# Optimization experiments

Hardware: AMD Instinct MI355X
Metric: run time of the kernel (lower is better)

Reference implementation:

```python
import jax, jax.numpy as jnp
import numpy as np

MODEL_DIM = 1024
NUM_HEADS = 16
HEAD_DIM = MODEL_DIM // NUM_HEADS
ROPE_THETA = 10000.0


def _rotate_half(x):
    x1, x2 = jnp.split(x, 2, axis=-1)
    return jnp.concatenate((-x2, x1), axis=-1)


def _rope_cos_sin(seq_len, dtype):
    inv_freq = 1.0 / (ROPE_THETA ** (jnp.arange(0, HEAD_DIM, 2, dtype=jnp.float32) / HEAD_DIM))
    pos = jnp.arange(seq_len, dtype=jnp.float32)
    freqs = jnp.einsum('i,j->ij', pos, inv_freq)  # [S, HEAD_DIM/2]
    emb = jnp.concatenate((freqs, freqs), axis=-1)  # [S, HEAD_DIM]
    return jnp.cos(emb).astype(dtype), jnp.sin(emb).astype(dtype)


def setup_inputs() -> dict:
    key = jax.random.key(0)
    ks = jax.random.split(key, 9)
    B, S, D = 4, 2048, MODEL_DIM
    scale = 1.0 / np.sqrt(D)
    inp = {
        'x': jax.random.normal(ks[0], (B, S, D), dtype=jnp.float32),
        'key_padding_mask': jnp.ones((B, S), dtype=bool),
        'wq': jax.random.normal(ks[1], (D, D), dtype=jnp.float32) * scale,
        'bq': jnp.zeros((D,), dtype=jnp.float32),
        'wk': jax.random.normal(ks[2], (D, D), dtype=jnp.float32) * scale,
        'bk': jnp.zeros((D,), dtype=jnp.float32),
        'wv': jax.random.normal(ks[3], (D, D), dtype=jnp.float32) * scale,
        'bv': jnp.zeros((D,), dtype=jnp.float32),
        'wo': jax.random.normal(ks[4], (D, D), dtype=jnp.float32) * scale,
        'bo': jnp.zeros((D,), dtype=jnp.float32),
    }
    return inp


def reference(x, key_padding_mask, wq, bq, wk, bk, wv, bv, wo, bo):
    B, S, D = x.shape
    H, Hd = NUM_HEADS, HEAD_DIM
    q = (x @ wq + bq).reshape(B, S, H, Hd).transpose(0, 2, 1, 3)
    k = (x @ wk + bk).reshape(B, S, H, Hd).transpose(0, 2, 1, 3)
    v = (x @ wv + bv).reshape(B, S, H, Hd).transpose(0, 2, 1, 3)
    cos, sin = _rope_cos_sin(S, x.dtype)  # [S, Hd]
    cos = cos[None, None]
    sin = sin[None, None]
    q = q * cos + _rotate_half(q) * sin
    k = k * cos + _rotate_half(k) * sin
    scores = jnp.einsum('bhqd,bhkd->bhqk', q, k) / jnp.sqrt(jnp.asarray(Hd, x.dtype))
    mask = key_padding_mask[:, None, None, :]
    scores = jnp.where(mask, scores, jnp.finfo(scores.dtype).min)
    attn = jax.nn.softmax(scores, axis=-1)
    ctx = jnp.einsum('bhqk,bhkd->bhqd', attn, v)
    ctx = ctx.transpose(0, 2, 1, 3).reshape(B, S, D)
    out = ctx @ wo + bo
    out = out * key_padding_mask[:, :, None].astype(out.dtype)
    return out
```

## Files before the change

### kernel.cpp

```cpp
#include <hip/hip_runtime.h>
#include <math.h>

#define S_LEN  2048
#define NH     16
#define HD     64
#define DMODEL 1024
#define BATCH  4
#define M_TOK  (BATCH * S_LEN)

typedef __bf16 bf16x8 __attribute__((ext_vector_type(8)));
typedef float  floatx4 __attribute__((ext_vector_type(4)));
typedef float  floatx16 __attribute__((ext_vector_type(16)));

typedef __attribute__((address_space(1))) const void cg_void;
typedef __attribute__((address_space(3))) void lds_void;

#if __has_builtin(__builtin_amdgcn_exp2f)
#define EXP2(x) __builtin_amdgcn_exp2f(x)
#else
#define EXP2(x) exp2f(x)
#endif

__device__ __forceinline__ void gload16(const void* g, void* l) {
    __builtin_amdgcn_global_load_lds((cg_void*)g, (lds_void*)l, 16, 0, 0);
}

__device__ __forceinline__ unsigned short f2bf(float f) {
    unsigned int u = __builtin_bit_cast(unsigned int, f);
    u = (u + 0x7FFF + ((u >> 16) & 1)) >> 16;
    return (unsigned short)u;
}

__device__ __forceinline__ unsigned cvtpk(float lo, float hi) {
    unsigned r;
    asm volatile("v_cvt_pk_bf16_f32 %0, %1, %2" : "=v"(r) : "v"(lo), "v"(hi));
    return r;
}

__device__ __forceinline__ void swap32(unsigned &a, unsigned &b) {
    asm volatile("v_permlane32_swap_b32 %0, %1" : "+v"(a), "+v"(b));
}

__device__ __forceinline__ float max3f(float a, float b, float c) {
    float r;
    asm("v_max3_f32 %0, %1, %2, %3" : "=v"(r) : "v"(a), "v"(b), "v"(c));
    return r;
}

__global__ __launch_bounds__(256)
void prep_kernel(const float* __restrict__ x,
                 const float* __restrict__ wq, const float* __restrict__ wk,
                 const float* __restrict__ wv, const float* __restrict__ wo,
                 const int* __restrict__ mask,
                 unsigned short* __restrict__ xb, unsigned short* __restrict__ wstack,
                 unsigned short* __restrict__ wto,
                 float* __restrict__ cs, float* __restrict__ sn,
                 float* __restrict__ biasG, int* __restrict__ flags)
{
    __shared__ float tile[32][33];
    const int blk = blockIdx.x;
    const int tid = threadIdx.x;
    constexpr size_t WSZ = (size_t)DMODEL * DMODEL;

    if (blk < 8192) {
        const int idx = blk * 256 + tid;
        float4 a = *reinterpret_cast<const float4*>(&x[(size_t)idx * 4]);
        ushort4 o;
        o.x = f2bf(a.x); o.y = f2bf(a.y); o.z = f2bf(a.z); o.w = f2bf(a.w);
        *reinterpret_cast<ushort4*>(&xb[(size_t)idx * 4]) = o;
    } else if (blk < 12288) {
        const int rel = blk - 8192;
        const int mat = rel >> 10;
        const float* w = (mat == 0) ? wq : (mat == 1) ? wk : (mat == 2) ? wv : wo;
        unsigned short* wt = (mat < 3) ? (wstack + (size_t)mat * WSZ) : wto;
        const int rel10 = rel & 1023;
        const int n0 = (rel10 & 31) * 32;
        const int k0 = (rel10 >> 5) * 32;
        const int tx  = tid & 31;
        const int ty8 = tid >> 5;
        #pragma unroll
        for (int i = 0; i < 4; ++i)
            tile[ty8 + i * 8][tx] = w[(size_t)(k0 + ty8 + i * 8) * DMODEL + n0 + tx];
        __syncthreads();
        #pragma unroll
        for (int i = 0; i < 4; ++i)
            wt[(size_t)(n0 + ty8 + i * 8) * DMODEL + k0 + tx] = f2bf(tile[tx][ty8 + i * 8]);
    } else if (blk < 12544) {
        const int idx = (blk - 12288) * 256 + tid;
        const int j = idx & 31;
        const int s = idx >> 5;
        double invf = pow(10000.0, -(double)j / 32.0);
        double a = (double)s * invf;
        cs[idx] = (float)cos(a);
        sn[idx] = (float)sin(a);
    } else {
        for (int i = tid; i < BATCH * S_LEN; i += 256) {
            const int b = i >> 11, r = i & 2047;
            const int kt = r >> 6, rem = r & 63;
            const int hig = rem >> 5, kbb = (rem >> 4) & 1, reg = rem & 15;
            const int key = kt * 64 + kbb * 32 + hig * 4 + (reg & 3) + ((reg >> 2) << 3);
            biasG[i] = mask[b * S_LEN + key] ? 0.0f : -3.0e38f;
        }
        for (int i = tid; i < BATCH * 32; i += 256) {
            const int b = i >> 5, kt = i & 31;
            int ok = 1;
            for (int j = 0; j < 64; ++j) ok &= (mask[b * S_LEN + kt * 64 + j] != 0);
            flags[i] = ok;
        }
    }
}

__global__ __launch_bounds__(256)
void gemm_qkv(const unsigned short* __restrict__ A, const unsigned short* __restrict__ Bt,
              const float* __restrict__ bq, const float* __restrict__ bk,
              const float* __restrict__ bv,
              const float* __restrict__ cs, const float* __restrict__ sn,
              unsigned short* __restrict__ qbf, unsigned short* __restrict__ kbf,
              unsigned short* __restrict__ vtb)
{
    constexpr int K = DMODEL;
    __shared__ unsigned short As[2][128 * 32];
    __shared__ unsigned short Bs[2][128 * 32];

    const int tid  = threadIdx.x;
    const int lane = tid & 63;
    const int w    = tid >> 6;
    const int wm   = w >> 1;
    const int wn   = w & 1;

    {
    }
    const int gx   = gridDim.x;
    int lin = blockIdx.y * gx + blockIdx.x;
    const int cpx = (gx * gridDim.y) >> 3;
    lin = (lin & 7) * cpx + (lin >> 3);
    const int row0 = (lin / gx) * 128;
    const int col0 = (lin % gx) * 128;

    const int sr  = lane >> 2;
    const int sk8 = (lane & 3) * 8;
    const int fr  = lane & 15;
    const int fk  = (lane >> 4) * 8;

    floatx4 acc[4][4] = {};

    #pragma unroll
    for (int t = 0; t < 2; ++t) {
        const int chunk = w * 32 + t * 16;
        gload16(A  + (size_t)(row0 + chunk + sr) * K + sk8, &As[0][chunk * 32]);
        gload16(Bt + (size_t)(col0 + chunk + sr) * K + sk8, &Bs[0][chunk * 32]);
    }

    for (int kt = 0; kt < K / 32; ++kt) {
        __syncthreads();
        if (kt + 1 < K / 32) {
            const int nb = (kt + 1) & 1;
            const int k0 = (kt + 1) * 32;
            #pragma unroll
            for (int t = 0; t < 2; ++t) {
                const int chunk = w * 32 + t * 16;
                gload16(A  + (size_t)(row0 + chunk + sr) * K + k0 + sk8, &As[nb][chunk * 32]);
                gload16(Bt + (size_t)(col0 + chunk + sr) * K + k0 + sk8, &Bs[nb][chunk * 32]);
            }
        }
        const int cur = kt & 1;
        bf16x8 av[4], bv4[4];
        #pragma unroll
        for (int m = 0; m < 4; ++m)
            av[m] = *reinterpret_cast<const bf16x8*>(&As[cur][(wm * 64 + m * 16 + fr) * 32 + fk]);
        #pragma unroll
        for (int n = 0; n < 4; ++n)
            bv4[n] = *reinterpret_cast<const bf16x8*>(&Bs[cur][(wn * 64 + n * 16 + fr) * 32 + fk]);
        #pragma unroll
        for (int m = 0; m < 4; ++m)
            #pragma unroll
            for (int n = 0; n < 4; ++n)
                acc[m][n] = __builtin_amdgcn_mfma_f32_16x16x32_bf16(av[m], bv4[n], acc[m][n], 0, 0, 0);
    }

    const int rbase = lane >> 4;
    const int sect  = col0 >> 10;
    const int c0    = col0 & 1023;

    if (sect == 2) {
        #pragma unroll
        for (int m = 0; m < 4; ++m)
            #pragma unroll
            for (int n = 0; n < 4; ++n) {
                const int c  = c0 + wn * 64 + n * 16 + fr;
                const int hh = c >> 6, d = c & 63;
                const int mr0 = row0 + wm * 64 + m * 16 + rbase * 4;
                const int bb = mr0 >> 11, ss = mr0 & (S_LEN - 1);
                const float bc = bv[c];
                ushort4 pk4;
                pk4.x = f2bf(acc[m][n][0] + bc);
                pk4.y = f2bf(acc[m][n][1] + bc);
                pk4.z = f2bf(acc[m][n][2] + bc);
                pk4.w = f2bf(acc[m][n][3] + bc);
                *reinterpret_cast<ushort4*>(
                    &vtb[((size_t)(bb * NH + hh) * HD + d) * S_LEN + ss]) = pk4;
            }
    } else {
        unsigned short* outp = sect ? kbf : qbf;
        const float* bias = sect ? bk : bq;
        const float sc = sect ? 1.0f : 0.125f * 1.44269504088896f;
        #pragma unroll
        for (int m = 0; m < 4; ++m)
            #pragma unroll
            for (int n = 0; n < 2; ++n) {
                const int c  = c0 + wn * 64 + n * 16 + fr;
                const int hh = c >> 6, d = c & 63;
                const float b1 = bias[c], b2 = bias[c + 32];
                #pragma unroll
                for (int r = 0; r < 4; ++r) {
                    const int mr = row0 + wm * 64 + m * 16 + rbase * 4 + r;
                    const int bb = mr >> 11, ss = mr & (S_LEN - 1);
                    const float v1 = acc[m][n][r] + b1;
                    const float v2 = acc[m][n + 2][r] + b2;
                    const float co = cs[ss * 32 + d];
                    const float si = sn[ss * 32 + d];
                    const size_t base = ((size_t)(bb * NH + hh) * S_LEN + ss) * HD + d;
                    outp[base]      = f2bf((v1 * co - v2 * si) * sc);
                    outp[base + 32] = f2bf((v2 * co + v1 * si) * sc);
                }
            }
    }
}

__global__ __launch_bounds__(256)
void attn_mfma2(const unsigned short* __restrict__ qbf,
                const unsigned short* __restrict__ kbf,
                const unsigned short* __restrict__ vtb,
                const float* __restrict__ biasG,
                const int* __restrict__ flags,
                unsigned short* __restrict__ ctxb)
{
    __shared__ unsigned short Ks[2][64 * 64];
    __shared__ unsigned short Vs[2][64 * 64];

    const int tid  = threadIdx.x;
    const int lane = tid & 63;
    const int w    = tid >> 6;
    const int bh   = blockIdx.x;
    const int b    = bh >> 4;
    const int h    = bh & 15;
    const int q0   = blockIdx.y * 128 + w * 32;
    const size_t hb = (size_t)bh * S_LEN * HD;

    const int lo5 = lane & 31;
    const int hi5 = lane >> 5;
    const int srow   = lane >> 3;
    const int schunk = (lane & 7) ^ srow;

    bf16x8 qf[4];
    #pragma unroll
    for (int ks = 0; ks < 4; ++ks)
        qf[ks] = *reinterpret_cast<const bf16x8*>(
            &qbf[hb + (size_t)(q0 + lo5) * HD + ks * 16 + hi5 * 8]);

    floatx16 oacc[2];
    #pragma unroll
    for (int v = 0; v < 2; ++v)
        #pragma unroll
        for (int i = 0; i < 16; ++i) oacc[v][i] = 0.0f;
    float mrow = -3.0e38f, lrow = 0.0f;

    #define STAGE(KT, BUF)                                                                  \
        _Pragma("unroll")                                                                   \
        for (int t = 0; t < 2; ++t) {                                                       \
            const int r0 = w * 16 + t * 8;                                                  \
            gload16(kbf + hb + (size_t)((KT) * 64 + r0 + srow) * HD + schunk * 8,           \
                    &Ks[BUF][r0 * 64]);                                                     \
            gload16(vtb + ((size_t)bh * HD + r0 + srow) * S_LEN + (KT) * 64 + schunk * 8,   \
                    &Vs[BUF][r0 * 64]);                                                     \
        }

    STAGE(0, 0)

    for (int kt = 0; kt < S_LEN / 64; ++kt) {
        __syncthreads();
        if (kt + 1 < S_LEN / 64) { STAGE(kt + 1, (kt + 1) & 1) }
        const int cur = kt & 1;

        floatx16 sacc[2];
        if (flags[b * 32 + kt]) {
            #pragma unroll
            for (int kb = 0; kb < 2; ++kb)
                #pragma unroll
                for (int i = 0; i < 16; ++i) sacc[kb][i] = 0.0f;
        } else {
            const float4* bp = reinterpret_cast<const float4*>(
                &biasG[(size_t)(b * 32 + kt) * 64 + hi5 * 32]);
            #pragma unroll
            for (int kb = 0; kb < 2; ++kb)
                #pragma unroll
                for (int t = 0; t < 4; ++t) {
                    const float4 b4 = bp[kb * 4 + t];
                    sacc[kb][t * 4 + 0] = b4.x; sacc[kb][t * 4 + 1] = b4.y;
                    sacc[kb][t * 4 + 2] = b4.z; sacc[kb][t * 4 + 3] = b4.w;
                }
        }

        __builtin_amdgcn_s_setprio(1);
        #pragma unroll
        for (int kb = 0; kb < 2; ++kb) {
            #pragma unroll
            for (int ks = 0; ks < 4; ++ks) {
                const bf16x8 ak = *reinterpret_cast<const bf16x8*>(
                    (const char*)&Ks[cur][0] + (kb * 32 + lo5) * 128 +
                    ((ks * 32 + hi5 * 16) ^ ((lo5 & 7) << 4)));
                sacc[kb] = __builtin_amdgcn_mfma_f32_32x32x16_bf16(ak, qf[ks], sacc[kb], 0, 0, 0);
            }
        }
        __builtin_amdgcn_s_setprio(0);

        float r0 = max3f(sacc[0][0],  sacc[0][1],  sacc[0][2]);
        float r1 = max3f(sacc[0][3],  sacc[0][4],  sacc[0][5]);
        float r2 = max3f(sacc[0][6],  sacc[0][7],  sacc[0][8]);
        float r3 = max3f(sacc[0][9],  sacc[0][10], sacc[0][11]);
        float r4 = max3f(sacc[0][12], sacc[0][13], sacc[0][14]);
        float r5 = max3f(sacc[1][0],  sacc[1][1],  sacc[1][2]);
        float r6 = max3f(sacc[1][3],  sacc[1][4],  sacc[1][5]);
        float r7 = max3f(sacc[1][6],  sacc[1][7],  sacc[1][8]);
        float r8 = max3f(sacc[1][9],  sacc[1][10], sacc[1][11]);
        float r9 = max3f(sacc[1][12], sacc[1][13], sacc[1][14]);
        float s1 = max3f(r0, r1, r2);
        float s2 = max3f(r3, r4, r5);
        float s3 = max3f(r6, r7, r8);
        float s4 = max3f(r9, sacc[0][15], sacc[1][15]);
        float pmax = fmaxf(max3f(s1, s2, s3), s4);
        pmax = fmaxf(pmax, __shfl_xor(pmax, 32));

        if (!__all(pmax <= mrow + 8.0f)) {
            const float mnew = fmaxf(mrow, pmax);
            const float fscale = EXP2(mrow - mnew);
            mrow = mnew;
            lrow *= fscale;
            #pragma unroll
            for (int v = 0; v < 2; ++v)
                #pragma unroll
                for (int i = 0; i < 16; ++i) oacc[v][i] *= fscale;
        }

        float rs0 = 0.0f, rs1 = 0.0f, rs2 = 0.0f, rs3 = 0.0f;
        #pragma unroll
        for (int kb = 0; kb < 2; ++kb)
            #pragma unroll
            for (int i = 0; i < 16; i += 4) {
                float p0 = EXP2(sacc[kb][i + 0] - mrow);
                float p1 = EXP2(sacc[kb][i + 1] - mrow);
                float p2 = EXP2(sacc[kb][i + 2] - mrow);
                float p3 = EXP2(sacc[kb][i + 3] - mrow);
                sacc[kb][i + 0] = p0; sacc[kb][i + 1] = p1;
                sacc[kb][i + 2] = p2; sacc[kb][i + 3] = p3;
                rs0 += p0; rs1 += p1; rs2 += p2; rs3 += p3;
            }
        float rs = (rs0 + rs1) + (rs2 + rs3);
        rs += __shfl_xor(rs, 32);
        lrow += rs;

        unsigned U0[8], U1[8];
        #pragma unroll
        for (int kb = 0; kb < 2; ++kb)
            #pragma unroll
            for (int s = 0; s < 4; ++s) {
                U0[kb * 4 + s] = cvtpk(sacc[kb][4 * s + 0], sacc[kb][4 * s + 1]);
                U1[kb * 4 + s] = cvtpk(sacc[kb][4 * s + 2], sacc[kb][4 * s + 3]);
            }
        union PF { unsigned u[4]; bf16x8 v; };
        PF pf[4];
        #pragma unroll
        for (int ks = 0; ks < 4; ++ks) {
            unsigned a0 = U0[2 * ks], b0 = U0[2 * ks + 1];
            swap32(a0, b0);
            unsigned a1 = U1[2 * ks], b1 = U1[2 * ks + 1];
            swap32(a1, b1);
            pf[ks].u[0] = a0; pf[ks].u[1] = a1;
            pf[ks].u[2] = b0; pf[ks].u[3] = b1;
        }

        __builtin_amdgcn_s_setprio(1);
        #pragma unroll
        for (int vb = 0; vb < 2; ++vb) {
            #pragma unroll
            for (int ks = 0; ks < 4; ++ks) {
                const bf16x8 av = *reinterpret_cast<const bf16x8*>(
                    (const char*)&Vs[cur][0] + (vb * 32 + lo5) * 128 +
                    ((ks * 32 + hi5 * 16) ^ ((lo5 & 7) << 4)));
                oacc[vb] = __builtin_amdgcn_mfma_f32_32x32x16_bf16(av, pf[ks].v, oacc[vb], 0, 0, 0);
            }
        }
        __builtin_amdgcn_s_setprio(0);
    }

    const float inv = 1.0f / lrow;
    unsigned short* dst = &ctxb[((size_t)b * S_LEN + q0 + lo5) * DMODEL + h * HD];
    #pragma unroll
    for (int vb = 0; vb < 2; ++vb)
        #pragma unroll
        for (int s = 0; s < 4; ++s) {
            const int d0 = vb * 32 + s * 8 + hi5 * 4;
            ushort4 o4;
            o4.x = f2bf(oacc[vb][4 * s + 0] * inv);
            o4.y = f2bf(oacc[vb][4 * s + 1] * inv);
            o4.z = f2bf(oacc[vb][4 * s + 2] * inv);
            o4.w = f2bf(oacc[vb][4 * s + 3] * inv);
            *reinterpret_cast<ushort4*>(&dst[d0]) = o4;
        }
    #undef STAGE
}

__global__ __launch_bounds__(256)
void gemm_out(const unsigned short* __restrict__ A, const unsigned short* __restrict__ Bt,
              const float* __restrict__ bias, const int* __restrict__ mask,
              float* __restrict__ C)
{
    constexpr int K = DMODEL;
    __shared__ unsigned short As[2][128 * 32];
    __shared__ unsigned short Bs[2][128 * 32];

    const int tid  = threadIdx.x;
    const int lane = tid & 63;
    const int w    = tid >> 6;
    const int wm   = w >> 1;
    const int wn   = w & 1;

    const int gx   = gridDim.x;
    int lin = blockIdx.y * gx + blockIdx.x;
    const int cpx = (gx * gridDim.y) >> 3;
    lin = (lin & 7) * cpx + (lin >> 3);
    const int row0 = (lin >> 3) * 128;
    const int col0 = (lin & 7) * 128;

    const int sr  = lane >> 2;
    const int sk8 = (lane & 3) * 8;
    const int fr  = lane & 15;
    const int fk  = (lane >> 4) * 8;

    floatx4 acc[4][4] = {};

    #pragma unroll
    for (int t = 0; t < 2; ++t) {
        const int chunk = w * 32 + t * 16;
        gload16(A  + (size_t)(row0 + chunk + sr) * K + sk8, &As[0][chunk * 32]);
        gload16(Bt + (size_t)(col0 + chunk + sr) * K + sk8, &Bs[0][chunk * 32]);
    }

    for (int kt = 0; kt < K / 32; ++kt) {
        __syncthreads();
        if (kt + 1 < K / 32) {
            const int nb = (kt + 1) & 1;
            const int k0 = (kt + 1) * 32;
            #pragma unroll
            for (int t = 0; t < 2; ++t) {
                const int chunk = w * 32 + t * 16;
                gload16(A  + (size_t)(row0 + chunk + sr) * K + k0 + sk8, &As[nb][chunk * 32]);
                gload16(Bt + (size_t)(col0 + chunk + sr) * K + k0 + sk8, &Bs[nb][chunk * 32]);
            }
        }
        const int cur = kt & 1;
        bf16x8 av[4], bv4[4];
        #pragma unroll
        for (int m = 0; m < 4; ++m)
            av[m] = *reinterpret_cast<const bf16x8*>(&As[cur][(wm * 64 + m * 16 + fr) * 32 + fk]);
        #pragma unroll
        for (int n = 0; n < 4; ++n)
            bv4[n] = *reinterpret_cast<const bf16x8*>(&Bs[cur][(wn * 64 + n * 16 + fr) * 32 + fk]);
        #pragma unroll
        for (int m = 0; m < 4; ++m)
            #pragma unroll
            for (int n = 0; n < 4; ++n)
                acc[m][n] = __builtin_amdgcn_mfma_f32_16x16x32_bf16(av[m], bv4[n], acc[m][n], 0, 0, 0);
    }

    const int rbase = lane >> 4;
    #pragma unroll
    for (int m = 0; m < 4; ++m)
        #pragma unroll
        for (int n = 0; n < 4; ++n) {
            const int c = col0 + wn * 64 + n * 16 + fr;
            const float bc = bias[c];
            #pragma unroll
            for (int r = 0; r < 4; ++r) {
                const int mr = row0 + wm * 64 + m * 16 + rbase * 4 + r;
                C[(size_t)mr * DMODEL + c] = mask[mr] ? (acc[m][n][r] + bc) : 0.0f;
            }
        }
}

extern "C" void kernel_launch(void* const* d_in, const int* in_sizes, int n_in,
                              void* d_out, int out_size, void* d_ws, size_t ws_size,
                              hipStream_t stream) {
    const float* x    = (const float*)d_in[0];
    const int*   mask = (const int*)d_in[1];
    const float* wq = (const float*)d_in[2];
    const float* bq = (const float*)d_in[3];
    const float* wk = (const float*)d_in[4];
    const float* bk = (const float*)d_in[5];
    const float* wv = (const float*)d_in[6];
    const float* bv = (const float*)d_in[7];
    const float* wo = (const float*)d_in[8];
    const float* bo = (const float*)d_in[9];
    float* out = (float*)d_out;

    const size_t QKV = (size_t)M_TOK * DMODEL;
    const size_t WSZ = (size_t)DMODEL * DMODEL;
    unsigned short* xb     = (unsigned short*)d_ws;
    unsigned short* wstack = xb + QKV;
    unsigned short* wto    = wstack + 3 * WSZ;
    unsigned short* qbf    = wto + WSZ;
    unsigned short* kbf    = qbf + QKV;
    unsigned short* vtb    = kbf + QKV;
    unsigned short* ctxb   = vtb + QKV;
    float* cs    = (float*)(ctxb + QKV);
    float* sn    = cs + (size_t)S_LEN * 32;
    float* biasG = sn + (size_t)S_LEN * 32;
    int*   flags = (int*)(biasG + (size_t)BATCH * S_LEN);

    prep_kernel<<<12545, 256, 0, stream>>>(x, wq, wk, wv, wo, mask,
                                           xb, wstack, wto, cs, sn, biasG, flags);

    dim3 qkvgrid(3 * DMODEL / 128, M_TOK / 128);
    gemm_qkv<<<qkvgrid, 256, 0, stream>>>(xb, wstack, bq, bk, bv, cs, sn, qbf, kbf, vtb);

    dim3 agrid(BATCH * NH, S_LEN / 128);
    attn_mfma2<<<agrid, 256, 0, stream>>>(qbf, kbf, vtb, biasG, flags, ctxb);

    dim3 ogrid(DMODEL / 128, M_TOK / 128);
    gemm_out<<<ogrid, 256, 0, stream>>>(ctxb, wto, bo, mask, out);
}
```

Before: 341.5 us.

## Use 512-thread attention blocks with 4-stage K/V pipeline and bitmask flags

The attention kernel now runs 8 waves per block covering 256 queries, so each K/V tile loaded into LDS is shared by twice as many query rows. The double buffer becomes a 4-deep ring with loads issued two tiles ahead and explicit vmcnt waits plus raw barriers in place of __syncthreads. Per-tile mask flags are packed into one 32-bit word per batch and read once. The RoPE table is computed in float instead of double, which is cheaper in the prep kernel but slightly less precise. The trade-offs are twice the LDS per block, a halved grid (fewer blocks to spread across CUs), and waitcnt counts that must match the outstanding loads exactly.

```diff
diff --git a/kernel.cpp b/kernel.cpp
--- a/kernel.cpp
+++ b/kernel.cpp
@@ -55,9 +55,10 @@
                  unsigned short* __restrict__ xb, unsigned short* __restrict__ wstack,
                  unsigned short* __restrict__ wto,
                  float* __restrict__ cs, float* __restrict__ sn,
-                 float* __restrict__ biasG, int* __restrict__ flags)
+                 float* __restrict__ biasG, unsigned* __restrict__ flagmask)
 {
     __shared__ float tile[32][33];
+    __shared__ unsigned fm[4];
     const int blk = blockIdx.x;
     const int tid = threadIdx.x;
     constexpr size_t WSZ = (size_t)DMODEL * DMODEL;
@@ -89,10 +90,10 @@
         const int idx = (blk - 12288) * 256 + tid;
         const int j = idx & 31;
         const int s = idx >> 5;
-        double invf = pow(10000.0, -(double)j / 32.0);
-        double a = (double)s * invf;
-        cs[idx] = (float)cos(a);
-        sn[idx] = (float)sin(a);
+        const float invf = exp2f(-(float)j * (13.287712379549449f / 32.0f));
+        const float a = (float)s * invf;
+        cs[idx] = cosf(a);
+        sn[idx] = sinf(a);
     } else {
         for (int i = tid; i < BATCH * S_LEN; i += 256) {
             const int b = i >> 11, r = i & 2047;
@@ -101,12 +102,16 @@
             const int key = kt * 64 + kbb * 32 + hig * 4 + (reg & 3) + ((reg >> 2) << 3);
             biasG[i] = mask[b * S_LEN + key] ? 0.0f : -3.0e38f;
         }
+        if (tid < 4) fm[tid] = 0;
+        __syncthreads();
         for (int i = tid; i < BATCH * 32; i += 256) {
             const int b = i >> 5, kt = i & 31;
             int ok = 1;
             for (int j = 0; j < 64; ++j) ok &= (mask[b * S_LEN + kt * 64 + j] != 0);
-            flags[i] = ok;
-        }
+            if (ok) atomicOr(&fm[b], 1u << kt);
+        }
+        __syncthreads();
+        if (tid < 4) flagmask[tid] = fm[tid];
     }
 }
 
@@ -128,8 +133,6 @@
     const int wm   = w >> 1;
     const int wn   = w & 1;
 
-    {
-    }
     const int gx   = gridDim.x;
     int lin = blockIdx.y * gx + blockIdx.x;
     const int cpx = (gx * gridDim.y) >> 3;
@@ -227,16 +230,16 @@
     }
 }
 
-__global__ __launch_bounds__(256)
-void attn_mfma2(const unsigned short* __restrict__ qbf,
+__global__ __launch_bounds__(512)
+void attn_mfma3(const unsigned short* __restrict__ qbf,
                 const unsigned short* __restrict__ kbf,
                 const unsigned short* __restrict__ vtb,
                 const float* __restrict__ biasG,
-                const int* __restrict__ flags,
+                const unsigned* __restrict__ flagmask,
                 unsigned short* __restrict__ ctxb)
 {
-    __shared__ unsigned short Ks[2][64 * 64];
-    __shared__ unsigned short Vs[2][64 * 64];
+    __shared__ unsigned short Ks[4][64 * 64];
+    __shared__ unsigned short Vs[4][64 * 64];
 
     const int tid  = threadIdx.x;
     const int lane = tid & 63;
@@ -244,13 +247,14 @@
     const int bh   = blockIdx.x;
     const int b    = bh >> 4;
     const int h    = bh & 15;
-    const int q0   = blockIdx.y * 128 + w * 32;
+    const int q0   = blockIdx.y * 256 + w * 32;
     const size_t hb = (size_t)bh * S_LEN * HD;
 
     const int lo5 = lane & 31;
     const int hi5 = lane >> 5;
     const int srow   = lane >> 3;
     const int schunk = (lane & 7) ^ srow;
+    const unsigned fl = flagmask[b];
 
     bf16x8 qf[4];
     #pragma unroll
@@ -265,25 +269,17 @@
         for (int i = 0; i < 16; ++i) oacc[v][i] = 0.0f;
     float mrow = -3.0e38f, lrow = 0.0f;
 
-    #define STAGE(KT, BUF)                                                                  \
-        _Pragma("unroll")                                                                   \
-        for (int t = 0; t < 2; ++t) {                                                       \
-            const int r0 = w * 16 + t * 8;                                                  \
-            gload16(kbf + hb + (size_t)((KT) * 64 + r0 + srow) * HD + schunk * 8,           \
-                    &Ks[BUF][r0 * 64]);                                                     \
-            gload16(vtb + ((size_t)bh * HD + r0 + srow) * S_LEN + (KT) * 64 + schunk * 8,   \
-                    &Vs[BUF][r0 * 64]);                                                     \
-        }
-
-    STAGE(0, 0)
-
-    for (int kt = 0; kt < S_LEN / 64; ++kt) {
-        __syncthreads();
-        if (kt + 1 < S_LEN / 64) { STAGE(kt + 1, (kt + 1) & 1) }
-        const int cur = kt & 1;
-
+    #define STAGE(KT, BUF) do {                                                             \
+        const int r0 = w * 8;                                                               \
+        gload16(kbf + hb + (size_t)((KT) * 64 + r0 + srow) * HD + schunk * 8,               \
+                &Ks[BUF][r0 * 64]);                                                         \
+        gload16(vtb + ((size_t)bh * HD + r0 + srow) * S_LEN + (KT) * 64 + schunk * 8,       \
+                &Vs[BUF][r0 * 64]);                                                         \
+    } while (0)
+
+    auto TILE = [&](int kt, int buf) {
         floatx16 sacc[2];
-        if (flags[b * 32 + kt]) {
+        if ((fl >> kt) & 1u) {
             #pragma unroll
             for (int kb = 0; kb < 2; ++kb)
                 #pragma unroll
@@ -307,7 +303,7 @@
             #pragma unroll
             for (int ks = 0; ks < 4; ++ks) {
                 const bf16x8 ak = *reinterpret_cast<const bf16x8*>(
-                    (const char*)&Ks[cur][0] + (kb * 32 + lo5) * 128 +
+                    (const char*)&Ks[buf][0] + (kb * 32 + lo5) * 128 +
                     ((ks * 32 + hi5 * 16) ^ ((lo5 & 7) << 4)));
                 sacc[kb] = __builtin_amdgcn_mfma_f32_32x32x16_bf16(ak, qf[ks], sacc[kb], 0, 0, 0);
             }
@@ -385,13 +381,32 @@
             #pragma unroll
             for (int ks = 0; ks < 4; ++ks) {
                 const bf16x8 av = *reinterpret_cast<const bf16x8*>(
-                    (const char*)&Vs[cur][0] + (vb * 32 + lo5) * 128 +
+                    (const char*)&Vs[buf][0] + (vb * 32 + lo5) * 128 +
                     ((ks * 32 + hi5 * 16) ^ ((lo5 & 7) << 4)));
                 oacc[vb] = __builtin_amdgcn_mfma_f32_32x32x16_bf16(av, pf[ks].v, oacc[vb], 0, 0, 0);
             }
         }
         __builtin_amdgcn_s_setprio(0);
-    }
+    };
+
+    STAGE(0, 0);
+    STAGE(1, 1);
+
+    for (int kt = 0; kt < 30; ++kt) {
+        STAGE(kt + 2, (kt + 2) & 3);
+        asm volatile("s_waitcnt vmcnt(4)" ::: "memory");
+        __builtin_amdgcn_s_barrier();
+        __builtin_amdgcn_sched_barrier(0);
+        TILE(kt, kt & 3);
+    }
+    asm volatile("s_waitcnt vmcnt(2)" ::: "memory");
+    __builtin_amdgcn_s_barrier();
+    __builtin_amdgcn_sched_barrier(0);
+    TILE(30, 30 & 3);
+    asm volatile("s_waitcnt vmcnt(0)" ::: "memory");
+    __builtin_amdgcn_s_barrier();
+    __builtin_amdgcn_sched_barrier(0);
+    TILE(31, 31 & 3);
 
     const float inv = 1.0f / lrow;
     unsigned short* dst = &ctxb[((size_t)b * S_LEN + q0 + lo5) * DMODEL + h * HD];
@@ -515,16 +530,16 @@
     float* cs    = (float*)(ctxb + QKV);
     float* sn    = cs + (size_t)S_LEN * 32;
     float* biasG = sn + (size_t)S_LEN * 32;
-    int*   flags = (int*)(biasG + (size_t)BATCH * S_LEN);
+    unsigned* flagmask = (unsigned*)(biasG + (size_t)BATCH * S_LEN);
 
     prep_kernel<<<12545, 256, 0, stream>>>(x, wq, wk, wv, wo, mask,
-                                           xb, wstack, wto, cs, sn, biasG, flags);
+                                           xb, wstack, wto, cs, sn, biasG, flagmask);
 
     dim3 qkvgrid(3 * DMODEL / 128, M_TOK / 128);
     gemm_qkv<<<qkvgrid, 256, 0, stream>>>(xb, wstack, bq, bk, bv, cs, sn, qbf, kbf, vtb);
 
-    dim3 agrid(BATCH * NH, S_LEN / 128);
-    attn_mfma2<<<agrid, 256, 0, stream>>>(qbf, kbf, vtb, biasG, flags, ctxb);
+    dim3 agrid(BATCH * NH, S_LEN / 256);
+    attn_mfma3<<<agrid, 512, 0, stream>>>(qbf, kbf, vtb, biasG, flagmask, ctxb);
 
     dim3 ogrid(DMODEL / 128, M_TOK / 128);
     gemm_out<<<ogrid, 256, 0, stream>>>(ctxb, wto, bo, mask, out);
```

Result: faster. 309.8 us (-9.3%).
